# Kernel tuning notes

Measured on AMD Instinct MI355X. Metric: run time of the kernel, lower is better.

Reference implementation:

```python
import jax, jax.numpy as jnp
from jax import lax
import numpy as np

B, T, F = 256, 256, 40
H, A, HORIZON = 256, 64, 60
D_SP = 192


def setup_inputs() -> dict:
    key = jax.random.key(0)
    ks = jax.random.split(key, 16)
    s = 0.05  # weight scale to keep activations stable
    return {
        'x': jax.random.normal(ks[0], (B, T, F), jnp.float32),
        'W_sp': jax.random.normal(ks[1], (F, D_SP), jnp.float32) * s,
        'b_sp': jnp.zeros((D_SP,), jnp.float32),
        'Wx_ef': jax.random.normal(ks[2], (D_SP, 4 * H), jnp.float32) * s,
        'Wh_ef': jax.random.normal(ks[3], (H, 4 * H), jnp.float32) * s,
        'b_ef': jnp.zeros((4 * H,), jnp.float32),
        'Wx_eb': jax.random.normal(ks[4], (D_SP, 4 * H), jnp.float32) * s,
        'Wh_eb': jax.random.normal(ks[5], (H, 4 * H), jnp.float32) * s,
        'b_eb': jnp.zeros((4 * H,), jnp.float32),
        'We': jax.random.normal(ks[6], (2 * H, A), jnp.float32) * s,
        'Wd': jax.random.normal(ks[7], (H, A), jnp.float32) * s,
        'v': jax.random.normal(ks[8], (A,), jnp.float32) * s,
        'Wx_d': jax.random.normal(ks[9], (1 + 2 * H, 4 * H), jnp.float32) * s,
        'Wh_d': jax.random.normal(ks[10], (H, 4 * H), jnp.float32) * s,
        'b_d': jnp.zeros((4 * H,), jnp.float32),
        'W_ih': jax.random.normal(ks[11], (2 * H, H), jnp.float32) * s,
        'b_ih': jnp.zeros((H,), jnp.float32),
        'W_ic': jax.random.normal(ks[12], (2 * H, H), jnp.float32) * s,
        'b_ic': jnp.zeros((H,), jnp.float32),
        'Wo': jax.random.normal(ks[13], (H, 1), jnp.float32) * s,
        'bo': jnp.zeros((1,), jnp.float32),
    }


def _lstm_cell(x_t, h, c, Wx, Wh, b):
    g = x_t @ Wx + h @ Wh + b
    i, f, gg, o = jnp.split(g, 4, axis=-1)  # torch gate order i,f,g,o
    c = jax.nn.sigmoid(f) * c + jax.nn.sigmoid(i) * jnp.tanh(gg)
    h = jax.nn.sigmoid(o) * jnp.tanh(c)
    return h, c


def _lstm_scan(xs_tbd, Wx, Wh, b):
    # xs_tbd: [T, B, D] -> hs [T, B, H]
    h0 = jnp.zeros((xs_tbd.shape[1], Wh.shape[0]), xs_tbd.dtype)
    c0 = jnp.zeros_like(h0)
    def step(carry, x_t):
        h, c = carry
        h, c = _lstm_cell(x_t, h, c, Wx, Wh, b)
        return (h, c), h
    _, hs = lax.scan(step, (h0, c0), xs_tbd)
    return hs


def reference(x, W_sp, b_sp, Wx_ef, Wh_ef, b_ef, Wx_eb, Wh_eb, b_eb,
              We, Wd, v, Wx_d, Wh_d, b_d, W_ih, b_ih, W_ic, b_ic, Wo, bo):
    # spatial encoder (stand-in for DeepLOBEncoder): [B,T,F] -> [B,T,192]
    h_spatial = x @ W_sp + b_sp
    xs = jnp.swapaxes(h_spatial, 0, 1)          # [T, B, 192]
    hs_f = _lstm_scan(xs, Wx_ef, Wh_ef, b_ef)    # [T, B, H]
    hs_b = _lstm_scan(xs[::-1], Wx_eb, Wh_eb, b_eb)[::-1]
    enc_out = jnp.swapaxes(jnp.concatenate([hs_f, hs_b], axis=-1), 0, 1)  # [B,T,2H]

    enc_mean = enc_out.mean(axis=1)
    dec_h = jnp.tanh(enc_mean @ W_ih + b_ih)     # [B, H]
    dec_c = jnp.tanh(enc_mean @ W_ic + b_ic)

    enc_proj = enc_out @ We                      # [B, T, A] precomputed (same math)
    prev_y = ((x[:, -1, 0] + x[:, -1, 2]) / 2.0)[:, None]  # ask_idx=0, bid_idx=2

    def dec_step(carry, _):
        h, c, py = carry
        e = jnp.tanh(enc_proj + (h @ Wd)[:, None, :])        # [B,T,A]
        scores = e @ v                                        # [B,T]
        w = jax.nn.softmax(scores, axis=1)
        context = jnp.einsum('bt,bth->bh', w, enc_out)        # [B,2H]
        dec_in = jnp.concatenate([py, context], axis=1)       # [B,1+2H]
        h, c = _lstm_cell(dec_in, h, c, Wx_d, Wh_d, b_d)
        y = h @ Wo + bo                                       # [B,1]
        return (h, c, lax.stop_gradient(y)), y[:, 0]

    _, ys = lax.scan(dec_step, (dec_h, dec_c, prev_y), None, length=HORIZON)
    return jnp.swapaxes(ys, 0, 1)  # [B, horizon]
```

## Files before the change

kernel.cpp:

```cpp
#include <hip/hip_runtime.h>
#include <cmath>

#define B_ 256
#define T_ 256
#define F_ 40
#define H_ 256
#define A_ 64
#define HOR_ 60
#define DSP_ 192
#define ENC_NBLK 128
#define GRP_SZ 16
#define WSTR 456
#define FPAD 32
#define ADLD 1024

typedef unsigned short u16;
typedef unsigned int u32;
typedef __attribute__((ext_vector_type(8))) short bf16x8;
typedef __attribute__((ext_vector_type(4))) float f32x4;
typedef __attribute__((ext_vector_type(8))) u32 u32x8;
typedef __attribute__((ext_vector_type(4))) u32 u32x4;

__device__ __forceinline__ float sigm(float x){ return 1.f/(1.f+expf(-x)); }

__device__ __forceinline__ u16 f2bf(float x){
  u32 u = __float_as_uint(x);
  u32 r = (u + 0x7FFFu + ((u>>16)&1u)) >> 16;
  return (u16)r;
}
__device__ __forceinline__ float bf2f(u16 h){ return __uint_as_float(((u32)h)<<16); }
__device__ __forceinline__ u32 packsplit(float x){
  u16 hi = f2bf(x);
  u16 lo = f2bf(x - bf2f(hi));
  return (u32)hi | ((u32)lo<<16);
}
__device__ __forceinline__ float unpack2f(u32 v){
  return __uint_as_float(v<<16) + __uint_as_float(v & 0xFFFF0000u);
}

__device__ __forceinline__ float wred_sum(float v){
  #pragma unroll
  for (int o=32;o>0;o>>=1) v += __shfl_xor(v,o);
  return v;
}
__device__ __forceinline__ float wred_max(float v){
  #pragma unroll
  for (int o=32;o>0;o>>=1) v = fmaxf(v,__shfl_xor(v,o));
  return v;
}

__device__ __forceinline__ void cnt_signal(int* c){
  __hip_atomic_fetch_add(c, 1, __ATOMIC_RELEASE, __HIP_MEMORY_SCOPE_AGENT);
}
__device__ __forceinline__ void cnt_wait(const int* c, int n, int tid){
  if (tid == 0){
    while (__hip_atomic_load(c, __ATOMIC_ACQUIRE, __HIP_MEMORY_SCOPE_AGENT) < n)
      __builtin_amdgcn_s_sleep(1);
  }
  __syncthreads();
}

__global__ void conv_w(const float* __restrict__ Wx, const float* __restrict__ Wh,
                       u16* __restrict__ hi, u16* __restrict__ lo,
                       int KX, int Ktot, int N){
  int idx = blockIdx.x*256 + threadIdx.x;
  if (idx >= N*Ktot) return;
  int n = idx / Ktot, k = idx - n*Ktot;
  float w = (k < KX) ? Wx[(size_t)k*N + n] : Wh[(size_t)(k-KX)*N + n];
  u16 h = f2bf(w);
  hi[idx] = h;
  lo[idx] = f2bf(w - bf2f(h));
}

__global__ __launch_bounds__(192) void spatial_proj(
    const float* __restrict__ x, const float* __restrict__ W, const float* __restrict__ bsp,
    u32* __restrict__ hsp32){
  __shared__ float Ws[40][192];
  __shared__ float xr[40];
  int t = blockIdx.x, tid = threadIdx.x;
  for (int i = tid; i < 40*192; i += 192){ int k = i/192, c = i-k*192; Ws[k][c] = W[i]; }
  float bb = bsp[tid];
  __syncthreads();
  for (int b=0; b<B_; b++){
    if (tid < 40) xr[tid] = x[((size_t)b*T_ + t)*F_ + tid];
    __syncthreads();
    float acc = bb;
    #pragma unroll
    for (int k=0;k<40;k++) acc += xr[k]*Ws[k][tid];
    hsp32[((size_t)t*B_ + b)*DSP_ + tid] = packsplit(acc);
    __syncthreads();
  }
}

__global__ __launch_bounds__(256) void enc_scan(
    const u32* __restrict__ hsp32,
    const u16* __restrict__ W_hi, const u16* __restrict__ W_lo,
    const float* __restrict__ b_ef, const float* __restrict__ b_eb,
    u32* __restrict__ hbuf, u32* __restrict__ eo32, int* __restrict__ bar)
{
  extern __shared__ u16 smem[];
  u16* Whi = smem;
  u16* Wlo = smem + 4*16*WSTR;
  const int bid = blockIdx.x;
  const int grp = bid & 7;
  const int nt  = bid >> 3;
  const int dir = grp >> 2;
  const int m0  = (grp & 3) * 64;
  const int u0  = nt * 16;
  const int tid = threadIdx.x;
  const int wave = tid >> 6, lane = tid & 63;
  const int lrow = lane & 15, kblk = lane >> 4;
  const int koff = kblk * 8;
  {
    const size_t wbase = ((size_t)dir*1024 + u0) * 448;
    for (int idx = tid; idx < 4*16*448; idx += 256){
      int g = idx / (16*448);
      int r = idx - g*(16*448);
      int j = r / 448;
      int k = r - j*448;
      size_t go = wbase + ((size_t)g*256 + j)*448 + k;
      Whi[(g*16 + j)*WSTR + k] = W_hi[go];
      Wlo[(g*16 + j)*WSTR + k] = W_lo[go];
    }
  }
  const float* bias = dir ? b_eb : b_ef;
  float bg4[4];
  #pragma unroll
  for (int g=0; g<4; g++) bg4[g] = bias[g*H_ + u0 + lrow];
  __syncthreads();

  const int mrow = m0 + wave*16;
  const int arow = mrow + lrow;
  u32* hP0 = hbuf + (size_t)dir*(B_*H_);
  u32* hP1 = hbuf + (size_t)(2+dir)*(B_*H_);
  int* gbar = bar + grp*T_;
  float c_reg[4] = {0.f,0.f,0.f,0.f};

  for (int s=0; s<T_; s++){
    const int t = dir ? (T_-1-s) : s;
    f32x4 acc[4] = {};
    const u32* abase = hsp32 + ((size_t)t*B_ + arow)*DSP_;
    #pragma unroll
    for (int ks=0; ks<6; ks++){
      int kb = ks*32 + koff;
      u32x8 la = *(const u32x8*)(abase + kb);
      bf16x8 ah, al;
      #pragma unroll
      for (int j=0;j<8;j++){ ah[j]=(short)(la[j]&0xFFFFu); al[j]=(short)(la[j]>>16); }
      #pragma unroll
      for (int g=0; g<4; g++){
        bf16x8 bh = *(const bf16x8*)(Whi + (g*16+lrow)*WSTR + kb);
        bf16x8 bl = *(const bf16x8*)(Wlo + (g*16+lrow)*WSTR + kb);
        acc[g] = __builtin_amdgcn_mfma_f32_16x16x32_bf16(ah, bh, acc[g], 0,0,0);
        acc[g] = __builtin_amdgcn_mfma_f32_16x16x32_bf16(ah, bl, acc[g], 0,0,0);
        acc[g] = __builtin_amdgcn_mfma_f32_16x16x32_bf16(al, bh, acc[g], 0,0,0);
      }
    }
    if (s > 0){
      if (tid == 0){
        while (__hip_atomic_load(&gbar[s-1], __ATOMIC_ACQUIRE, __HIP_MEMORY_SCOPE_AGENT) < GRP_SZ)
          __builtin_amdgcn_s_sleep(1);
      }
      __syncthreads();
    }
    const u32* hin = (s & 1) ? hP1 : hP0;
    u32* hout      = (s & 1) ? hP0 : hP1;
    const u32* hbase = hin + (size_t)arow*H_;
    #pragma unroll
    for (int ks=0; ks<8; ks++){
      int kb = ks*32 + koff;
      u32x8 la = *(const u32x8*)(hbase + kb);
      bf16x8 ah, al;
      #pragma unroll
      for (int j=0;j<8;j++){ ah[j]=(short)(la[j]&0xFFFFu); al[j]=(short)(la[j]>>16); }
      #pragma unroll
      for (int g=0; g<4; g++){
        bf16x8 bh = *(const bf16x8*)(Whi + (g*16+lrow)*WSTR + 192 + kb);
        bf16x8 bl = *(const bf16x8*)(Wlo + (g*16+lrow)*WSTR + 192 + kb);
        acc[g] = __builtin_amdgcn_mfma_f32_16x16x32_bf16(ah, bh, acc[g], 0,0,0);
        acc[g] = __builtin_amdgcn_mfma_f32_16x16x32_bf16(ah, bl, acc[g], 0,0,0);
        acc[g] = __builtin_amdgcn_mfma_f32_16x16x32_bf16(al, bh, acc[g], 0,0,0);
      }
    }
    #pragma unroll
    for (int r=0; r<4; r++){
      int brow = mrow + kblk*4 + r;
      float gi = acc[0][r] + bg4[0];
      float gf = acc[1][r] + bg4[1];
      float gg = acc[2][r] + bg4[2];
      float go = acc[3][r] + bg4[3];
      float cn = sigm(gf)*c_reg[r] + sigm(gi)*tanhf(gg);
      float hn = sigm(go)*tanhf(cn);
      c_reg[r] = cn;
      u32 hp = packsplit(hn);
      hout[(size_t)brow*H_ + u0 + lrow] = hp;
      eo32[((size_t)brow*T_ + t)*512 + dir*H_ + u0 + lrow] = hp;
    }
    if (s == T_-1) break;
    __syncthreads();
    if (tid == 0)
      __hip_atomic_fetch_add(&gbar[s], 1, __ATOMIC_RELEASE, __HIP_MEMORY_SCOPE_AGENT);
  }
}

__global__ __launch_bounds__(512) void dec_scan(
    const u32* __restrict__ eo32,
    const u16* __restrict__ Wet_hi, const u16* __restrict__ Wet_lo,
    const float* __restrict__ W_ih, const float* __restrict__ b_ih,
    const float* __restrict__ W_ic, const float* __restrict__ b_ic,
    const float* __restrict__ x, float* __restrict__ ep,
    const float* __restrict__ Wd, const float* __restrict__ v,
    const float* __restrict__ Wo, const float* __restrict__ bo,
    const u16* __restrict__ W_hi, const u16* __restrict__ W_lo,
    const float* __restrict__ b_d, const float* __restrict__ Wx_d,
    float* __restrict__ hdp, float* __restrict__ cd,
    u32* __restrict__ Ad32, float* __restrict__ py,
    float* __restrict__ out, int* __restrict__ cntA, int* __restrict__ cntB)
{
  __shared__ float sh_h[256], sh_hwd[64], sh_v[64], sh_sc[256], sh_w[256];
  __shared__ float red8[8][64];
  __shared__ float sh_red[4], sh_red2[4];
  __shared__ float redc[8][512];
  __shared__ float gl[4][16][16];
  __shared__ float em_s[512];
  const int b = blockIdx.x, tid = threadIdx.x;
  const int wave = tid >> 6, lane = tid & 63;
  const int bx = b & 15, by = b >> 4;
  const int cr = tid >> 4, cu = tid & 15;
  float c_reg = 0.f;
  float bg0=0,bg1=0,bg2=0,bg3=0, w00=0,w01=0,w02=0,w03=0;
  if (tid < 256){
    int uu = bx*16 + cu;
    bg0 = b_d[uu];       bg1 = b_d[256+uu];
    bg2 = b_d[512+uu];   bg3 = b_d[768+uu];
    w00 = Wx_d[uu];      w01 = Wx_d[256+uu];
    w02 = Wx_d[512+uu];  w03 = Wx_d[768+uu];
  }
  {
    const int lrow = lane & 15, kblk = lane >> 4, koff = kblk*8;
    #pragma unroll
    for (int mi=0; mi<2; mi++){
      int mt = wave*2 + mi;
      f32x4 acc[4] = {};
      for (int ks=0; ks<16; ks++){
        int kb = ks*32 + koff;
        u32x8 ld = *(const u32x8*)(eo32 + ((size_t)b*T_ + mt*16 + lrow)*512 + kb);
        bf16x8 ah, al;
        #pragma unroll
        for (int j=0;j<8;j++){ ah[j]=(short)(ld[j]&0xFFFFu); al[j]=(short)(ld[j]>>16); }
        #pragma unroll
        for (int nf=0; nf<4; nf++){
          bf16x8 bh = *(const bf16x8*)(Wet_hi + (size_t)(nf*16+lrow)*512 + kb);
          bf16x8 bl = *(const bf16x8*)(Wet_lo + (size_t)(nf*16+lrow)*512 + kb);
          acc[nf] = __builtin_amdgcn_mfma_f32_16x16x32_bf16(ah, bh, acc[nf], 0,0,0);
          acc[nf] = __builtin_amdgcn_mfma_f32_16x16x32_bf16(ah, bl, acc[nf], 0,0,0);
          acc[nf] = __builtin_amdgcn_mfma_f32_16x16x32_bf16(al, bh, acc[nf], 0,0,0);
        }
      }
      #pragma unroll
      for (int nf=0; nf<4; nf++)
        #pragma unroll
        for (int r=0; r<4; r++)
          ep[((size_t)b*T_ + mt*16 + kblk*4 + r)*64 + nf*16 + lrow] = acc[nf][r];
    }
  }
  {
    float cacc[8] = {};
    const u32* eo = eo32 + (size_t)b*T_*512 + lane*8;
    #pragma unroll 8
    for (int tt=0; tt<32; tt++){
      int t = wave*32 + tt;
      u32x4 e0 = *(const u32x4*)(eo + (size_t)t*512);
      u32x4 e1 = *(const u32x4*)(eo + (size_t)t*512 + 4);
      #pragma unroll
      for (int j=0;j<4;j++){ cacc[j] += unpack2f(e0[j]); cacc[4+j] += unpack2f(e1[j]); }
    }
    #pragma unroll
    for (int j=0;j<8;j++) redc[wave][lane*8+j] = cacc[j];
    __syncthreads();
    if (tid < 256){
      float s0=0.f, s1=0.f;
      #pragma unroll
      for (int q=0;q<8;q++){ s0 += redc[q][tid]; s1 += redc[q][256+tid]; }
      em_s[tid] = s0*(1.f/T_); em_s[256+tid] = s1*(1.f/T_);
    }
    __syncthreads();
  }
  if (tid < 256){
    float ah = b_ih[tid], ac = b_ic[tid];
    for (int k=0;k<512;k++){
      float e = em_s[k];
      ah += e*W_ih[(size_t)k*256 + tid];
      ac += e*W_ic[(size_t)k*256 + tid];
    }
    float h0 = tanhf(ah), c0 = tanhf(ac);
    sh_h[tid] = h0;
    hdp[(size_t)b*H_ + tid] = h0;
    Ad32[(size_t)b*ADLD + 512 + tid] = packsplit(h0);
    cd[(size_t)b*H_ + tid] = c0;
  }
  if (tid == 0){
    size_t xb = ((size_t)b*T_ + 255)*F_;
    py[b] = (x[xb] + x[xb+2])*0.5f;
  }
  if (tid >= 448) sh_v[tid-448] = v[tid-448];
  __syncthreads();
  for (int s=0; s<=HOR_; s++){
    if (s > 0){
      cnt_wait(cntB + (size_t)((s-1)*16 + by)*FPAD, 16, tid);
      if (tid < 256) sh_h[tid] = hdp[(size_t)(s&1)*B_*H_ + (size_t)b*H_ + tid];
      __syncthreads();
      if (tid < 256){
        float p = sh_h[tid] * Wo[tid];
        p = wred_sum(p);
        if ((tid & 63) == 0) sh_red[tid>>6] = p;
      }
      __syncthreads();
      if (tid == 0){
        float y = sh_red[0]+sh_red[1]+sh_red[2]+sh_red[3] + bo[0];
        out[b*HOR_ + (s-1)] = y;
        py[b] = y;
      }
    }
    if (s == HOR_) break;
    {
      float ssum = 0.f;
      for (int j=wave*32; j<wave*32+32; j++) ssum += sh_h[j]*Wd[(size_t)j*A_ + lane];
      red8[wave][lane] = ssum;
      __syncthreads();
      if (tid < 64){
        float a = 0.f;
        #pragma unroll
        for (int q=0;q<8;q++) a += red8[q][tid];
        sh_hwd[tid] = a;
      }
    }
    __syncthreads();
    {
      int t = tid >> 1, aa = tid & 1;
      const float4* ep4 = (const float4*)(ep + ((size_t)(b*T_+t))*A_ + aa*32);
      float partial = 0.f;
      #pragma unroll
      for (int q=0;q<8;q++){
        float4 e4 = ep4[q];
        int a0 = aa*32 + q*4;
        partial += tanhf(e4.x + sh_hwd[a0+0]) * sh_v[a0+0];
        partial += tanhf(e4.y + sh_hwd[a0+1]) * sh_v[a0+1];
        partial += tanhf(e4.z + sh_hwd[a0+2]) * sh_v[a0+2];
        partial += tanhf(e4.w + sh_hwd[a0+3]) * sh_v[a0+3];
      }
      partial += __shfl_xor(partial, 1);
      if (aa == 0) sh_sc[t] = partial;
    }
    __syncthreads();
    if (tid < 256){
      float sc = sh_sc[tid];
      float m = wred_max(sc);
      if ((tid&63)==0) sh_red[tid>>6] = m;
      __syncthreads();
      m = fmaxf(fmaxf(sh_red[0],sh_red[1]), fmaxf(sh_red[2],sh_red[3]));
      float e = expf(sc - m);
      float su = wred_sum(e);
      if ((tid&63)==0) sh_red2[tid>>6] = su;
      __syncthreads();
      su = (sh_red2[0]+sh_red2[1])+(sh_red2[2]+sh_red2[3]);
      sh_w[tid] = e / su;
    } else { __syncthreads(); __syncthreads(); }
    __syncthreads();
    {
      float cacc[8] = {};
      const u32* eo = eo32 + (size_t)b*T_*512 + lane*8;
      #pragma unroll 8
      for (int tt=0; tt<32; tt++){
        int t = wave*32 + tt;
        float wgt = sh_w[t];
        u32x4 e0 = *(const u32x4*)(eo + (size_t)t*512);
        u32x4 e1 = *(const u32x4*)(eo + (size_t)t*512 + 4);
        #pragma unroll
        for (int j=0;j<4;j++){
          cacc[j]   += wgt * unpack2f(e0[j]);
          cacc[4+j] += wgt * unpack2f(e1[j]);
        }
      }
      #pragma unroll
      for (int j=0;j<8;j++) redc[wave][lane*8+j] = cacc[j];
    }
    __syncthreads();
    if (tid < 256){
      float c0 = 0.f, c1 = 0.f;
      #pragma unroll
      for (int q=0;q<8;q++){ c0 += redc[q][tid]; c1 += redc[q][256+tid]; }
      Ad32[(size_t)b*ADLD + tid]       = packsplit(c0);
      Ad32[(size_t)b*ADLD + 256 + tid] = packsplit(c1);
    }
    __syncthreads();
    if (tid == 0)
      cnt_signal(cntA + (size_t)(s*16 + by)*FPAD);
    cnt_wait(cntA + (size_t)(s*16 + by)*FPAD, 16, tid);
    if (s == 0 && tid < 256)
      c_reg = cd[(size_t)(by*16 + cr)*H_ + bx*16 + cu];
    const int par = s & 1;
    if (wave < 4){
      const int g = wave;
      const int r16 = lane & 15, kb4 = lane >> 4;
      f32x4 acc = {0.f,0.f,0.f,0.f};
      const u32* ar = Ad32 + (size_t)(by*16 + r16)*ADLD;
      const u16* WH = W_hi + (size_t)(g*256 + bx*16 + r16)*768;
      const u16* WL = W_lo + (size_t)(g*256 + bx*16 + r16)*768;
      for (int ks=0; ks<24; ks++){
        int kb = ks*32 + kb4*8;
        int kp = (kb < 512) ? kb : (kb + (par<<8));
        u32x8 ld = *(const u32x8*)(ar + kp);
        bf16x8 ah, al;
        #pragma unroll
        for (int j=0;j<8;j++){ ah[j]=(short)(ld[j]&0xFFFFu); al[j]=(short)(ld[j]>>16); }
        bf16x8 bh = *(const bf16x8*)(WH + kb);
        bf16x8 bl = *(const bf16x8*)(WL + kb);
        acc = __builtin_amdgcn_mfma_f32_16x16x32_bf16(ah, bh, acc, 0,0,0);
        acc = __builtin_amdgcn_mfma_f32_16x16x32_bf16(ah, bl, acc, 0,0,0);
        acc = __builtin_amdgcn_mfma_f32_16x16x32_bf16(al, bh, acc, 0,0,0);
      }
      #pragma unroll
      for (int vv=0; vv<4; vv++) gl[g][kb4*4+vv][r16] = acc[vv];
    }
    __syncthreads();
    if (tid < 256){
      float pyr = py[by*16 + cr];
      float gi = gl[0][cr][cu] + bg0 + pyr*w00;
      float gf = gl[1][cr][cu] + bg1 + pyr*w01;
      float gg = gl[2][cr][cu] + bg2 + pyr*w02;
      float go = gl[3][cr][cu] + bg3 + pyr*w03;
      float cn = sigm(gf)*c_reg + sigm(gi)*tanhf(gg);
      float hn = sigm(go)*tanhf(cn);
      c_reg = cn;
      size_t ridx = (size_t)(by*16+cr)*H_ + bx*16+cu;
      hdp[(size_t)((s+1)&1)*B_*H_ + ridx] = hn;
      Ad32[(size_t)(by*16+cr)*ADLD + 512 + (((s+1)&1)<<8) + bx*16+cu] = packsplit(hn);
    }
    __syncthreads();
    if (tid == 0)
      cnt_signal(cntB + (size_t)(s*16 + by)*FPAD);
  }
}

extern "C" void kernel_launch(void* const* d_in, const int* in_sizes, int n_in,
                              void* d_out, int out_size, void* d_ws, size_t ws_size,
                              hipStream_t stream)
{
  const float* x    = (const float*)d_in[0];
  const float* W_sp = (const float*)d_in[1];
  const float* b_sp = (const float*)d_in[2];
  const float* Wx_ef= (const float*)d_in[3];
  const float* Wh_ef= (const float*)d_in[4];
  const float* b_ef = (const float*)d_in[5];
  const float* Wx_eb= (const float*)d_in[6];
  const float* Wh_eb= (const float*)d_in[7];
  const float* b_eb = (const float*)d_in[8];
  const float* We   = (const float*)d_in[9];
  const float* Wd   = (const float*)d_in[10];
  const float* v    = (const float*)d_in[11];
  const float* Wx_d = (const float*)d_in[12];
  const float* Wh_d = (const float*)d_in[13];
  const float* b_d  = (const float*)d_in[14];
  const float* W_ih = (const float*)d_in[15];
  const float* b_ih = (const float*)d_in[16];
  const float* W_ic = (const float*)d_in[17];
  const float* b_ic = (const float*)d_in[18];
  const float* Wo   = (const float*)d_in[19];
  const float* bo   = (const float*)d_in[20];
  float* out = (float*)d_out;

  char* base = (char*)d_ws;
  auto alloc = [&](size_t bytes)->char*{
    char* p = base; base += (bytes + 255) & ~(size_t)255; return p;
  };
  u16* Wenc_hi = (u16*)alloc((size_t)2*1024*448*2);
  u16* Wenc_lo = (u16*)alloc((size_t)2*1024*448*2);
  u16* Wdec_hi = (u16*)alloc((size_t)1024*768*2);
  u16* Wdec_lo = (u16*)alloc((size_t)1024*768*2);
  u16* Wet_hi  = (u16*)alloc((size_t)64*512*2);
  u16* Wet_lo  = (u16*)alloc((size_t)64*512*2);
  u32* hsp32   = (u32*)alloc((size_t)T_*B_*DSP_*4);
  u32* hbuf    = (u32*)alloc((size_t)2*2*B_*H_*4);
  u32* eo32    = (u32*)alloc((size_t)B_*T_*512*4);
  float* ep    = (float*)alloc((size_t)B_*T_*64*4);
  float* cd    = (float*)alloc((size_t)B_*H_*4);
  float* hdp   = (float*)alloc((size_t)2*B_*H_*4);
  u32* Ad32    = (u32*)alloc((size_t)B_*ADLD*4);
  float* pyb   = (float*)alloc((size_t)B_*4);
  int* bar     = (int*)alloc((size_t)8*T_*4);
  int* cntA    = (int*)alloc((size_t)HOR_*16*FPAD*4);
  int* cntB    = (int*)alloc((size_t)HOR_*16*FPAD*4);
  if ((size_t)(base - (char*)d_ws) > ws_size) return;

  conv_w<<<dim3(1792),256,0,stream>>>(Wx_ef, Wh_ef, Wenc_hi, Wenc_lo, DSP_, 448, 1024);
  conv_w<<<dim3(1792),256,0,stream>>>(Wx_eb, Wh_eb, Wenc_hi+458752, Wenc_lo+458752, DSP_, 448, 1024);
  conv_w<<<dim3(3072),256,0,stream>>>(Wx_d+1024, Wh_d, Wdec_hi, Wdec_lo, 512, 768, 1024);
  conv_w<<<dim3(128),256,0,stream>>>(We, We, Wet_hi, Wet_lo, 512, 512, 64);

  spatial_proj<<<dim3(256),192,0,stream>>>(x, W_sp, b_sp, hsp32);

  hipMemsetAsync(hbuf, 0, (size_t)2*B_*H_*4, stream);
  hipMemsetAsync(bar, 0, (size_t)8*T_*4, stream);
  hipMemsetAsync(cntA, 0, (size_t)HOR_*16*FPAD*4, stream);
  hipMemsetAsync(cntB, 0, (size_t)HOR_*16*FPAD*4, stream);

  enc_scan<<<dim3(ENC_NBLK), dim3(256), 2*4*16*WSTR*2, stream>>>(
      hsp32, Wenc_hi, Wenc_lo, b_ef, b_eb, hbuf, eo32, bar);

  dec_scan<<<dim3(256),512,0,stream>>>(
      eo32, Wet_hi, Wet_lo, W_ih, b_ih, W_ic, b_ic, x, ep,
      Wd, v, Wo, bo, Wdec_hi, Wdec_lo, b_d, Wx_d,
      hdp, cd, Ad32, pyb, out, cntA, cntB);
}
```

Measured before the change: 5.767 ms.

## Cache leading encoder rows in LDS and split decoder gate GEMM across all waves

Each decoder block now copies the first CT=56 timesteps of its encoder output (packed hi/lo bf16) into shared memory once. In every decode step the context reduction reads those rows from LDS instead of global memory, and falls back to global loads for the rest. The gate GEMM is also split along K between the two halves of the 8 waves, so all waves issue MFMAs instead of only four, and the two partial sums are added in the gate stage. The cost is about 115KB more LDS per block, which may limit occupancy or exceed LDS limits, plus an extra gate reduction through shared memory.

```diff
diff --git a/kernel.cpp b/kernel.cpp
--- a/kernel.cpp
+++ b/kernel.cpp
@@ -13,6 +13,7 @@
 #define WSTR 456
 #define FPAD 32
 #define ADLD 1024
+#define CT 56
 
 typedef unsigned short u16;
 typedef unsigned int u32;
@@ -221,8 +222,9 @@
   __shared__ float red8[8][64];
   __shared__ float sh_red[4], sh_red2[4];
   __shared__ float redc[8][512];
-  __shared__ float gl[4][16][16];
+  __shared__ float gl[8][16][16];
   __shared__ float em_s[512];
+  __shared__ u32 eoL[CT*512];
   const int b = blockIdx.x, tid = threadIdx.x;
   const int wave = tid >> 6, lane = tid & 63;
   const int bx = b & 15, by = b >> 4;
@@ -235,6 +237,11 @@
     bg2 = b_d[512+uu];   bg3 = b_d[768+uu];
     w00 = Wx_d[uu];      w01 = Wx_d[256+uu];
     w02 = Wx_d[512+uu];  w03 = Wx_d[768+uu];
+  }
+  {
+    const u32* src = eo32 + (size_t)b*T_*512;
+    for (int i = tid; i < CT*512/4; i += 512)
+      ((u32x4*)eoL)[i] = *(const u32x4*)(src + (size_t)i*4);
   }
   {
     const int lrow = lane & 15, kblk = lane >> 4, koff = kblk*8;
@@ -369,10 +376,23 @@
     __syncthreads();
     {
       float cacc[8] = {};
+      const int t0 = wave*32, t1 = t0 + 32;
+      const int tL = (t1 < CT) ? t1 : CT;
+      for (int t=t0; t<tL; ++t){
+        float wgt = sh_w[t];
+        const u32* p = eoL + t*512 + lane*8;
+        u32x4 e0 = *(const u32x4*)p;
+        u32x4 e1 = *(const u32x4*)(p + 4);
+        #pragma unroll
+        for (int j=0;j<4;j++){
+          cacc[j]   += wgt * unpack2f(e0[j]);
+          cacc[4+j] += wgt * unpack2f(e1[j]);
+        }
+      }
       const u32* eo = eo32 + (size_t)b*T_*512 + lane*8;
-      #pragma unroll 8
-      for (int tt=0; tt<32; tt++){
-        int t = wave*32 + tt;
+      const int tG = (t0 > CT) ? t0 : CT;
+      #pragma unroll 4
+      for (int t=tG; t<t1; ++t){
         float wgt = sh_w[t];
         u32x4 e0 = *(const u32x4*)(eo + (size_t)t*512);
         u32x4 e1 = *(const u32x4*)(eo + (size_t)t*512 + 4);
@@ -400,14 +420,14 @@
     if (s == 0 && tid < 256)
       c_reg = cd[(size_t)(by*16 + cr)*H_ + bx*16 + cu];
     const int par = s & 1;
-    if (wave < 4){
-      const int g = wave;
+    {
+      const int g = wave & 3, kh = wave >> 2;
       const int r16 = lane & 15, kb4 = lane >> 4;
       f32x4 acc = {0.f,0.f,0.f,0.f};
       const u32* ar = Ad32 + (size_t)(by*16 + r16)*ADLD;
       const u16* WH = W_hi + (size_t)(g*256 + bx*16 + r16)*768;
       const u16* WL = W_lo + (size_t)(g*256 + bx*16 + r16)*768;
-      for (int ks=0; ks<24; ks++){
+      for (int ks=kh*12; ks<kh*12+12; ks++){
         int kb = ks*32 + kb4*8;
         int kp = (kb < 512) ? kb : (kb + (par<<8));
         u32x8 ld = *(const u32x8*)(ar + kp);
@@ -421,15 +441,15 @@
         acc = __builtin_amdgcn_mfma_f32_16x16x32_bf16(al, bh, acc, 0,0,0);
       }
       #pragma unroll
-      for (int vv=0; vv<4; vv++) gl[g][kb4*4+vv][r16] = acc[vv];
+      for (int vv=0; vv<4; vv++) gl[wave][kb4*4+vv][r16] = acc[vv];
     }
     __syncthreads();
     if (tid < 256){
       float pyr = py[by*16 + cr];
-      float gi = gl[0][cr][cu] + bg0 + pyr*w00;
-      float gf = gl[1][cr][cu] + bg1 + pyr*w01;
-      float gg = gl[2][cr][cu] + bg2 + pyr*w02;
-      float go = gl[3][cr][cu] + bg3 + pyr*w03;
+      float gi = gl[0][cr][cu] + gl[4][cr][cu] + bg0 + pyr*w00;
+      float gf = gl[1][cr][cu] + gl[5][cr][cu] + bg1 + pyr*w01;
+      float gg = gl[2][cr][cu] + gl[6][cr][cu] + bg2 + pyr*w02;
+      float go = gl[3][cr][cu] + gl[7][cr][cu] + bg3 + pyr*w03;
       float cn = sigm(gf)*c_reg + sigm(gi)*tanhf(gg);
       float hn = sigm(go)*tanhf(cn);
       c_reg = cn;
```

New measurement: 5.555 ms. 1.04x faster.
